# Kernel tuning notes

Hardware: AMD Instinct MI355X
Metric: run time of the kernel (lower is better)

Reference implementation:

```python
import jax, jax.numpy as jnp
import numpy as np

K = 20
EPS = 1e-5
NEG_SLOPE = 0.2


def _graph_feature(x, k):
    # x: [B, N, C] -> edge features [B, N, k, 2C]
    xx = jnp.sum(x * x, axis=-1)                       # [B, N]
    inner = jnp.einsum('bnc,bmc->bnm', x, x)           # [B, N, N]
    neg_dist = 2.0 * inner - xx[:, :, None] - xx[:, None, :]
    idx = jax.lax.top_k(neg_dist, k)[1]                # [B, N, k] nearest neighbors
    nbr = jax.vmap(lambda f, i: f[i])(x, idx)          # [B, N, k, C]
    center = jnp.broadcast_to(x[:, :, None, :], nbr.shape)
    return jnp.concatenate([nbr - center, center], axis=-1)


def _bn(y, gamma, beta, axes):
    mu = y.mean(axes, keepdims=True)
    var = y.var(axes, keepdims=True)
    return (y - mu) * jax.lax.rsqrt(var + EPS) * gamma + beta


def _lrelu(y):
    return jnp.where(y > 0, y, NEG_SLOPE * y)


def _edge_block(feat, w, gamma, beta):
    # feat: [B, N, k, Cin], w: [Cout, Cin] (1x1 conv)
    y = jnp.einsum('bnkc,oc->bnko', feat, w)
    y = _lrelu(_bn(y, gamma, beta, (0, 1, 2)))
    return y.max(axis=2)                               # max over k -> [B, N, Cout]


def setup_inputs() -> dict:
    key = jax.random.key(0)
    ks = jax.random.split(key, 8)
    B, N = 16, 2048
    num_features = 128
    x = jax.random.normal(ks[0], (B, N, 3), dtype=jnp.float32)
    s = 0.05
    w1 = jax.random.normal(ks[1], (64, 6), dtype=jnp.float32) * s
    w2 = jax.random.normal(ks[2], (64, 128), dtype=jnp.float32) * s
    w3 = jax.random.normal(ks[3], (128, 128), dtype=jnp.float32) * s
    w4 = jax.random.normal(ks[4], (256, 256), dtype=jnp.float32) * s
    w5 = jax.random.normal(ks[5], (512, 512), dtype=jnp.float32) * s
    we = jax.random.normal(ks[6], (num_features, 512), dtype=jnp.float32) * s
    def gb(c):
        return jnp.ones((c,), jnp.float32), jnp.zeros((c,), jnp.float32)
    g1, b1 = gb(64); g2, b2 = gb(64); g3, b3 = gb(128); g4, b4 = gb(256); g5, b5 = gb(512)
    return dict(x=x, w1=w1, g1=g1, b1=b1, w2=w2, g2=g2, b2=b2, w3=w3, g3=g3, b3=b3,
                w4=w4, g4=g4, b4=b4, w5=w5, g5=g5, b5=b5, we=we)


def reference(x, w1, g1, b1, w2, g2, b2, w3, g3, b3, w4, g4, b4, w5, g5, b5, we):
    # x: [B, N, 3]
    x1 = _edge_block(_graph_feature(x, K), w1, g1, b1)    # [B, N, 64]
    x2 = _edge_block(_graph_feature(x1, K), w2, g2, b2)   # [B, N, 64]
    x3 = _edge_block(_graph_feature(x2, K), w3, g3, b3)   # [B, N, 128]
    x4 = _edge_block(_graph_feature(x3, K), w4, g4, b4)   # [B, N, 256]
    cat = jnp.concatenate([x1, x2, x3, x4], axis=-1)      # [B, N, 512]
    y = jnp.einsum('bnc,oc->bno', cat, w5)                # conv5 (1x1 conv1d)
    y = _lrelu(_bn(y, g5, b5, (0, 1)))
    y = y.max(axis=1)                                     # global max pool -> [B, 512]
    return y @ we.T                                       # embedding -> [B, num_features]
```

## Files before the change

### kernel.cpp

```cpp
#include <hip/hip_runtime.h>
#include <hip/hip_bf16.h>
#include <cstdint>

#define B_ 16
#define N_ 2048
#define KNN_K 20
#define EPS_ 1e-5f
#define SLOPE_ 0.2f

typedef __attribute__((ext_vector_type(4))) float f32x4;
typedef __attribute__((ext_vector_type(8))) short bf16x8;

static __device__ __forceinline__ float lrelu(float v){ return v > 0.f ? v : SLOPE_*v; }

static __device__ __forceinline__ unsigned encf(float f){
  unsigned b = __float_as_uint(f);
  return (b & 0x80000000u) ? ~b : (b | 0x80000000u);
}
static __device__ __forceinline__ float decf(unsigned u){
  unsigned b = (u & 0x80000000u) ? (u ^ 0x80000000u) : ~u;
  return __uint_as_float(b);
}
static __device__ __forceinline__ short bfbits(float v){
  __hip_bfloat16 h = __float2bfloat16(v);
  return *reinterpret_cast<short*>(&h);
}
static __device__ __forceinline__ float bf2f(short s){
  __hip_bfloat16 h = *reinterpret_cast<__hip_bfloat16*>(&s);
  return __bfloat162float(h);
}

template<int C, int CP>
__global__ __launch_bounds__(256) void convert_kernel(const float* __restrict__ f, int lda,
                                                      short* __restrict__ fbf, size_t plane,
                                                      float* __restrict__ xx){
  int wid  = (blockIdx.x * 256 + threadIdx.x) >> 6;
  int lane = threadIdx.x & 63;
  if (wid >= B_*N_) return;
  const float* p = f + (size_t)wid*lda;
  float s = 0.f;
  for (int c = lane; c < CP; c += 64){
    float v = (c < C) ? p[c] : 0.f;
    short h = bfbits(v);
    float r1 = v - bf2f(h);
    short m = bfbits(r1);
    short l = bfbits(r1 - bf2f(m));
    size_t o = (size_t)wid*CP + c;
    fbf[o] = h;
    fbf[plane + o] = m;
    fbf[2*plane + o] = l;
    s += v*v;
  }
  #pragma unroll
  for (int off=32; off; off>>=1) s += __shfl_down(s, off);
  if (lane==0) xx[wid] = s;
}

template<int CP>
__global__ __launch_bounds__(256, (CP==128)?3:4) void knn_mfma(const short* __restrict__ fbf, size_t plane,
                                                const float* __restrict__ xx,
                                                float* __restrict__ pval, int* __restrict__ pidx){
  constexpr int SP = CP + 8;
  constexpr int CH = CP/8;
  constexpr int KC = CP/32;
  constexpr int PF = 3*CP/32;
  constexpr int FMBS = 3*64*SP;
  constexpr bool ALIAS = (FMBS*2 >= 64*65*4);
  constexpr unsigned LDSB = ALIAS ? (unsigned)(FMBS*2) : (unsigned)(FMBS*2 + 64*65*4);
  __shared__ __align__(16) char ldsbuf[LDSB];
  short* fmb = (short*)ldsbuf;
  float* dtile = ALIAS ? (float*)ldsbuf : (float*)(ldsbuf + FMBS*2);
  __shared__ float xn_s[64], xm_s[64];

  int b   = blockIdx.x >> 6;
  int rem = blockIdx.x & 63;
  int n0  = (rem >> 1) << 6;
  int mh  = rem & 1;
  int mbase = mh << 10;
  int tid = threadIdx.x;
  int w    = tid >> 6;
  int lane = tid & 63;
  int fr = lane & 15, hi = lane >> 4;
  int r_loc = lane >> 2, csub = lane & 3;
  int gb = lane & 60;
  int myrow = w*16 + r_loc;
  size_t browoff = (size_t)b * N_;

  bf16x8 aH[KC], aM[KC], aL[KC];
  {
    size_t arow = (browoff + n0 + w*16 + fr) * (size_t)CP;
    #pragma unroll
    for (int kc=0; kc<KC; ++kc){
      aH[kc] = *(const bf16x8*)&fbf[arow + kc*32 + hi*8];
      aM[kc] = *(const bf16x8*)&fbf[plane + arow + kc*32 + hi*8];
      aL[kc] = *(const bf16x8*)&fbf[2*plane + arow + kc*32 + hi*8];
    }
  }
  if (tid < 64) xn_s[tid] = xx[browoff + n0 + tid];

  float sv[5]; int si[5];
  #pragma unroll
  for (int j=0;j<5;++j){ sv[j] = -1e30f; si[j] = 0x7FFFFFFF; }

  bf16x8 pf[PF];
  float xmreg = 0.f;
  auto PFLOAD = [&](int mt){
    int m0 = mbase + (mt<<6);
    #pragma unroll
    for (int j=0;j<PF;++j){
      int i = tid + j*256;
      int p = i/(64*CH); int rm = i - p*64*CH; int r = rm/CH, cq = rm - r*CH;
      pf[j] = *(const bf16x8*)&fbf[(size_t)p*plane + (browoff + m0 + r)*(size_t)CP + cq*8];
    }
    if (tid < 64) xmreg = xx[browoff + m0 + tid];
  };
  auto WRITEPF = [&](){
    #pragma unroll
    for (int j=0;j<PF;++j){
      int i = tid + j*256;
      int p = i/(64*CH); int rm = i - p*64*CH; int r = rm/CH, cq = rm - r*CH;
      *(bf16x8*)&fmb[p*64*SP + r*SP + cq*8] = pf[j];
    }
    if (tid < 64) xm_s[tid] = xmreg;
  };

  PFLOAD(0);
  WRITEPF();
  __syncthreads();

  for (int mt = 0; mt < 16; ++mt){
    int m0 = mbase + (mt << 6);
    if (mt + 1 < 16) PFLOAD(mt + 1);

    f32x4 acc[4];
    #pragma unroll
    for (int ct=0; ct<4; ++ct) acc[ct] = (f32x4){0.f,0.f,0.f,0.f};
    const short* BH = fmb;
    const short* BM = fmb + 64*SP;
    const short* BL = fmb + 2*64*SP;
    #pragma unroll
    for (int kc = 0; kc < KC; ++kc){
      #pragma unroll
      for (int ct=0; ct<4; ++ct){
        int boff = (ct*16 + fr)*SP + kc*32 + hi*8;
        bf16x8 bh = *(const bf16x8*)&BH[boff];
        bf16x8 bm = *(const bf16x8*)&BM[boff];
        bf16x8 bl = *(const bf16x8*)&BL[boff];
        acc[ct] = __builtin_amdgcn_mfma_f32_16x16x32_bf16(aH[kc], bh, acc[ct], 0,0,0);
        acc[ct] = __builtin_amdgcn_mfma_f32_16x16x32_bf16(aM[kc], bh, acc[ct], 0,0,0);
        acc[ct] = __builtin_amdgcn_mfma_f32_16x16x32_bf16(aH[kc], bm, acc[ct], 0,0,0);
        acc[ct] = __builtin_amdgcn_mfma_f32_16x16x32_bf16(aM[kc], bm, acc[ct], 0,0,0);
        acc[ct] = __builtin_amdgcn_mfma_f32_16x16x32_bf16(aL[kc], bh, acc[ct], 0,0,0);
        acc[ct] = __builtin_amdgcn_mfma_f32_16x16x32_bf16(aH[kc], bl, acc[ct], 0,0,0);
      }
    }
    __syncthreads();

    #pragma unroll
    for (int reg=0; reg<4; ++reg){
      int nl = w*16 + hi*4 + reg;
      float xn = xn_s[nl];
      #pragma unroll
      for (int ct=0; ct<4; ++ct)
        dtile[nl*65 + ct*16 + fr] = 2.f*acc[ct][reg] - xn - xm_s[ct*16 + fr];
    }

    int base = myrow*65 + csub*16;
    float thr = __shfl(sv[4], lane | 3);
    unsigned qm = 0u;
    #pragma unroll
    for (int jj=0; jj<16; ++jj){
      float v = dtile[base + jj];
      qm |= (v > thr) ? (1u << jj) : 0u;
    }
    unsigned long long bal = __ballot(qm != 0u);
    while (bal){
      unsigned nib = (unsigned)((bal >> gb) & 0xFull);
      int leader = nib ? (gb + (int)__builtin_ctz(nib)) : 64;
      int bbit = (int)__builtin_ctz(qm | 0x10000u);
      float mv = dtile[base + (bbit & 15)];
      int mid = m0 + (csub << 4) + bbit;
      float cv = __shfl(mv, leader);
      int   cid = __shfl(mid, leader);
      qm = (lane == leader) ? (qm & (qm - 1u)) : qm;
      int cnt = 0;
      #pragma unroll
      for (int j=0;j<5;++j) cnt += (sv[j] >= cv) ? 1 : 0;
      cnt += __shfl_xor(cnt, 1);
      cnt += __shfl_xor(cnt, 2);
      int pos = nib ? cnt : 20;
      float pv = __shfl_up(sv[4], 1);
      int   pi = __shfl_up(si[4], 1);
      #pragma unroll
      for (int j=0;j<5;++j){
        int g = csub*5 + j;
        float ns = (g < pos) ? sv[j] : ((g == pos) ? cv : pv);
        int   ni = (g < pos) ? si[j] : ((g == pos) ? cid : pi);
        pv = sv[j]; pi = si[j];
        sv[j] = ns; si[j] = ni;
      }
      bal = __ballot(qm != 0u);
    }

    if (mt + 1 < 16){
      if constexpr (ALIAS){
        __syncthreads();
        WRITEPF();
        __syncthreads();
      } else {
        WRITEPF();
        __syncthreads();
      }
    }
  }

  size_t orow = browoff + n0 + myrow;
  float* pvo = pval + (orow*2 + mh)*KNN_K + csub*5;
  int*   pio = pidx + (orow*2 + mh)*KNN_K + csub*5;
  #pragma unroll
  for (int j=0;j<5;++j){ pvo[j] = sv[j]; pio[j] = si[j]; }
}

__global__ __launch_bounds__(256) void knn_merge(const float* __restrict__ pval,
                                                 const int* __restrict__ pidx,
                                                 int* __restrict__ idxout){
  int r = blockIdx.x*256 + threadIdx.x;
  if (r >= B_*N_) return;
  const float* va = pval + (size_t)r*2*KNN_K;
  const float* vb = va + KNN_K;
  const int*   ia = pidx + (size_t)r*2*KNN_K;
  const int*   ib = ia + KNN_K;
  int i=0, j=0;
  #pragma unroll
  for (int t=0;t<KNN_K;++t){
    float a = va[i], bq = vb[j];
    bool ta = (a >= bq);
    idxout[(size_t)r*KNN_K + t] = ta ? ia[i] : ib[j];
    i += ta ? 1 : 0; j += ta ? 0 : 1;
  }
}

template<int CP>
__global__ __launch_bounds__(256) void gemm_pq(const short* __restrict__ fbf, size_t plane,
                                               const float* __restrict__ Wsrc, int wstride, int Cin,
                                               float* __restrict__ Out, int O){
  constexpr int BK = (CP < 64) ? CP : 64;
  constexpr int SP = BK + 8;
  __shared__ short Ah[128*SP];
  __shared__ short Am[128*SP];
  __shared__ short Wh[64*SP];
  __shared__ short Wm[64*SP];
  int obl = O >> 6;
  int bo = ((int)blockIdx.x % obl) << 6;
  int bm = ((int)blockIdx.x / obl) << 7;
  int tid = threadIdx.x;
  int w = tid >> 6, lane = tid & 63;
  int fr = lane & 15, hi = lane >> 4;
  f32x4 acc[2][4];
  #pragma unroll
  for (int g=0; g<2; ++g)
    #pragma unroll
    for (int ct=0; ct<4; ++ct) acc[g][ct] = (f32x4){0.f,0.f,0.f,0.f};

  for (int k0=0; k0<CP; k0+=BK){
    __syncthreads();
    for (int i=tid; i < 128*(BK/8); i += 256){
      int r = i/(BK/8), cq = i%(BK/8);
      size_t src = ((size_t)bm + r)*CP + k0 + cq*8;
      *(bf16x8*)&Ah[r*SP + cq*8] = *(const bf16x8*)&fbf[src];
      *(bf16x8*)&Am[r*SP + cq*8] = *(const bf16x8*)&fbf[plane + src];
    }
    for (int i=tid; i < 64*(BK/8); i += 256){
      int r = i/(BK/8), cq = i%(BK/8);
      bf16x8 vh, vm;
      #pragma unroll
      for (int e=0;e<8;++e){
        int c = k0 + cq*8 + e;
        float v = (c < Cin) ? Wsrc[(size_t)(bo + r)*wstride + c] : 0.f;
        short h = bfbits(v);
        vh[e] = h;
        vm[e] = bfbits(v - bf2f(h));
      }
      *(bf16x8*)&Wh[r*SP + cq*8] = vh;
      *(bf16x8*)&Wm[r*SP + cq*8] = vm;
    }
    __syncthreads();
    #pragma unroll
    for (int kc=0; kc<BK/32; ++kc){
      bf16x8 a0h = *(const bf16x8*)&Ah[(w*32 +      fr)*SP + kc*32 + hi*8];
      bf16x8 a0m = *(const bf16x8*)&Am[(w*32 +      fr)*SP + kc*32 + hi*8];
      bf16x8 a1h = *(const bf16x8*)&Ah[(w*32 + 16 + fr)*SP + kc*32 + hi*8];
      bf16x8 a1m = *(const bf16x8*)&Am[(w*32 + 16 + fr)*SP + kc*32 + hi*8];
      #pragma unroll
      for (int ct=0; ct<4; ++ct){
        bf16x8 bh = *(const bf16x8*)&Wh[(ct*16 + fr)*SP + kc*32 + hi*8];
        bf16x8 bm = *(const bf16x8*)&Wm[(ct*16 + fr)*SP + kc*32 + hi*8];
        acc[0][ct] = __builtin_amdgcn_mfma_f32_16x16x32_bf16(a0h, bh, acc[0][ct], 0,0,0);
        acc[0][ct] = __builtin_amdgcn_mfma_f32_16x16x32_bf16(a0m, bh, acc[0][ct], 0,0,0);
        acc[0][ct] = __builtin_amdgcn_mfma_f32_16x16x32_bf16(a0h, bm, acc[0][ct], 0,0,0);
        acc[1][ct] = __builtin_amdgcn_mfma_f32_16x16x32_bf16(a1h, bh, acc[1][ct], 0,0,0);
        acc[1][ct] = __builtin_amdgcn_mfma_f32_16x16x32_bf16(a1m, bh, acc[1][ct], 0,0,0);
        acc[1][ct] = __builtin_amdgcn_mfma_f32_16x16x32_bf16(a1h, bm, acc[1][ct], 0,0,0);
      }
    }
  }
  #pragma unroll
  for (int g=0; g<2; ++g)
    #pragma unroll
    for (int ct=0; ct<4; ++ct)
      #pragma unroll
      for (int reg=0; reg<4; ++reg){
        int row = bm + w*32 + g*16 + hi*4 + reg;
        Out[(size_t)row*O + bo + ct*16 + fr] = acc[g][ct][reg];
      }
}

__global__ __launch_bounds__(256) void gemm_bf16(const float* __restrict__ A,
                                                 const float* __restrict__ Wt,
                                                 float* __restrict__ C){
  __shared__ short As[128*72];
  __shared__ short Bs[64*72];
  int bm = (int)(blockIdx.x >> 3) << 7;
  int bo = (int)(blockIdx.x & 7) << 6;
  int tid = threadIdx.x;
  int w = tid >> 6, lane = tid & 63;
  int fr = lane & 15, hi = lane >> 4;
  f32x4 acc[2][4];
  #pragma unroll
  for (int g=0; g<2; ++g)
    #pragma unroll
    for (int ct=0; ct<4; ++ct) acc[g][ct] = (f32x4){0.f,0.f,0.f,0.f};

  for (int k0=0; k0<512; k0+=64){
    __syncthreads();
    #pragma unroll 2
    for (int i = tid; i < 1024; i += 256){
      int r = i >> 3, cq = i & 7;
      const float* src = &A[(size_t)(bm + r)*512 + k0 + cq*8];
      bf16x8 v;
      #pragma unroll
      for (int e=0;e<8;++e) v[e] = bfbits(src[e]);
      *(bf16x8*)&As[r*72 + cq*8] = v;
    }
    #pragma unroll 2
    for (int i = tid; i < 512; i += 256){
      int r = i >> 3, cq = i & 7;
      const float* src = &Wt[(size_t)(bo + r)*512 + k0 + cq*8];
      bf16x8 v;
      #pragma unroll
      for (int e=0;e<8;++e) v[e] = bfbits(src[e]);
      *(bf16x8*)&Bs[r*72 + cq*8] = v;
    }
    __syncthreads();
    #pragma unroll
    for (int kc=0; kc<2; ++kc){
      bf16x8 a0 = *(const bf16x8*)&As[(w*32 +      fr)*72 + kc*32 + hi*8];
      bf16x8 a1 = *(const bf16x8*)&As[(w*32 + 16 + fr)*72 + kc*32 + hi*8];
      #pragma unroll
      for (int ct=0; ct<4; ++ct){
        bf16x8 bb = *(const bf16x8*)&Bs[(ct*16 + fr)*72 + kc*32 + hi*8];
        acc[0][ct] = __builtin_amdgcn_mfma_f32_16x16x32_bf16(a0, bb, acc[0][ct], 0,0,0);
        acc[1][ct] = __builtin_amdgcn_mfma_f32_16x16x32_bf16(a1, bb, acc[1][ct], 0,0,0);
      }
    }
  }
  #pragma unroll
  for (int g=0; g<2; ++g)
    #pragma unroll
    for (int ct=0; ct<4; ++ct)
      #pragma unroll
      for (int reg=0; reg<4; ++reg){
        int row = bm + w*32 + g*16 + hi*4 + reg;
        C[(size_t)row*512 + bo + ct*16 + fr] = acc[g][ct][reg];
      }
}

__global__ void wq_kernel(const float* __restrict__ w, float* __restrict__ wq, int Cin, int O){
  int i = blockIdx.x*blockDim.x + threadIdx.x;
  if (i >= O*Cin) return;
  int o = i / Cin, c = i - o*Cin;
  wq[i] = w[(size_t)o*2*Cin + Cin + c] - w[(size_t)o*2*Cin + c];
}

__global__ void zero_f_kernel(float* p, int n){
  int i = blockIdx.x*blockDim.x + threadIdx.x;
  if (i < n) p[i] = 0.f;
}
__global__ void zero_u_kernel(unsigned* p, int n){
  int i = blockIdx.x*blockDim.x + threadIdx.x;
  if (i < n) p[i] = 0u;
}

__global__ __launch_bounds__(256) void edge_agg(const float* __restrict__ P, const float* __restrict__ Q,
      const int* __restrict__ idx, const float* __restrict__ gamma,
      float* __restrict__ S, float* __restrict__ sums, float* __restrict__ sumsq, int O){
  const int ROWS = 64;
  int rpi = 256 / O;
  int iters = ROWS / rpi;
  int row0 = blockIdx.x * ROWS;
  int tid = threadIdx.x;
  int o  = tid % O;
  int rl = tid / O;
  int b  = row0 / N_;
  __shared__ int sidx[4][KNN_K];
  __shared__ float s1[256], s2[256];
  float g = gamma[o];
  float csum=0.f, csumsq=0.f;
  for (int it=0; it<iters; ++it){
    __syncthreads();
    if (tid < KNN_K*rpi) sidx[tid/KNN_K][tid%KNN_K] = idx[(size_t)(row0 + it*rpi)*KNN_K + tid];
    __syncthreads();
    int row = row0 + it*rpi + rl;
    float q = Q[(size_t)row*O + o];
    float mx=-1e30f, mn=1e30f, s=0.f, ss=0.f;
    #pragma unroll
    for (int k=0;k<KNN_K;++k){
      int m = sidx[rl][k];
      float p = P[((size_t)b*N_ + m)*O + o];
      mx = fmaxf(mx,p); mn = fminf(mn,p);
      float y = p + q; s += y; ss += y*y;
    }
    csum += s; csumsq += ss;
    S[(size_t)row*O + o] = (g >= 0.f ? mx : mn) + q;
  }
  s1[tid]=0.f; s2[tid]=0.f;
  __syncthreads();
  atomicAdd(&s1[o], csum); atomicAdd(&s2[o], csumsq);
  __syncthreads();
  if (tid < O){ atomicAdd(&sums[tid], s1[tid]); atomicAdd(&sumsq[tid], s2[tid]); }
}

__global__ void bn_finalize(const float* __restrict__ sums, const float* __restrict__ sumsq,
                            const float* __restrict__ gamma, const float* __restrict__ beta,
                            float invM, float* __restrict__ scale, float* __restrict__ shift, int O){
  int o = blockIdx.x*blockDim.x + threadIdx.x;
  if (o >= O) return;
  float mu = sums[o]*invM;
  float var = sumsq[o]*invM - mu*mu;
  float rs = rsqrtf(var + EPS_);
  float sc = gamma[o]*rs;
  scale[o] = sc; shift[o] = beta[o] - mu*sc;
}

__global__ void apply_write(const float* __restrict__ S, const float* __restrict__ scale,
                            const float* __restrict__ shift, float* __restrict__ cat, int off, int O){
  int i = blockIdx.x*blockDim.x + threadIdx.x;
  if (i >= B_*N_*O) return;
  int row = i / O, o = i - row*O;
  float v = S[i]*scale[o] + shift[o];
  cat[(size_t)row*512 + off + o] = lrelu(v);
}

__global__ __launch_bounds__(256) void conv5_stats(const float* __restrict__ Y, const float* __restrict__ g5,
      float* __restrict__ sums, float* __restrict__ sumsq, unsigned* __restrict__ maxenc){
  int bb = blockIdx.x / 16;
  int n0 = (blockIdx.x % 16) * 128;
  int tid = threadIdx.x;
  float s0=0.f, s1=0.f, q0=0.f, q1=0.f, m0=-1e30f, m1=-1e30f;
  float ga = g5[tid], gb = g5[tid+256];
  for (int n=0;n<128;++n){
    size_t base = ((size_t)bb*N_ + n0 + n)*512;
    float ya = Y[base + tid];
    float yb = Y[base + tid + 256];
    s0 += ya; q0 += ya*ya;
    s1 += yb; q1 += yb*yb;
    m0 = fmaxf(m0, ga>=0.f ? ya : -ya);
    m1 = fmaxf(m1, gb>=0.f ? yb : -yb);
  }
  atomicAdd(&sums[tid],      s0); atomicAdd(&sumsq[tid],      q0);
  atomicAdd(&sums[tid+256],  s1); atomicAdd(&sumsq[tid+256],  q1);
  atomicMax(&maxenc[bb*512 + tid],       encf(m0));
  atomicMax(&maxenc[bb*512 + tid + 256], encf(m1));
}

__global__ void pool_kernel(const unsigned* __restrict__ maxenc, const float* __restrict__ scale,
                            const float* __restrict__ shift, const float* __restrict__ g5,
                            float* __restrict__ pooled){
  int i = blockIdx.x*blockDim.x + threadIdx.x;
  if (i >= B_*512) return;
  int o = i & 511;
  float t = decf(maxenc[i]);
  float y = g5[o] >= 0.f ? t : -t;
  pooled[i] = lrelu(y*scale[o] + shift[o]);
}

__global__ void final_mm(const float* __restrict__ pooled, const float* __restrict__ we,
                         float* __restrict__ out){
  int i = blockIdx.x*blockDim.x + threadIdx.x;
  if (i >= B_*128) return;
  int b = i >> 7, j = i & 127;
  const float4* pp = (const float4*)(pooled + (size_t)b*512);
  const float4* wp = (const float4*)(we + (size_t)j*512);
  float s = 0.f;
  for (int c=0;c<128;++c){
    float4 a = pp[c], w = wp[c];
    s += a.x*w.x + a.y*w.y + a.z*w.z + a.w*w.w;
  }
  out[i] = s;
}

struct Ws {
  float* cat; float* P; float* Q; float* S; int* idx; float* xx;
  float* sums; float* sumsq; float* scale; float* shift;
  float* wq; unsigned* maxenc; float* pooled; short* fbf;
  float* pval; int* pidx;
};

template<int C, int CP>
static void run_layer(const Ws& W, const float* f, int lda, int O,
                      const float* w, const float* g, const float* bt,
                      int off_out, hipStream_t stream){
  const int M = B_*N_;
  size_t plane = (size_t)M*CP;
  convert_kernel<C, CP><<<M/4, 256, 0, stream>>>(f, lda, W.fbf, plane, W.xx);
  knn_mfma<CP><<<B_*(N_/64)*2, 256, 0, stream>>>(W.fbf, plane, W.xx, W.pval, W.pidx);
  knn_merge<<<(M+255)/256, 256, 0, stream>>>(W.pval, W.pidx, W.idx);
  int nwq = O*C;
  wq_kernel<<<(nwq+255)/256, 256, 0, stream>>>(w, W.wq, C, O);
  int grid = (M/128)*(O/64);
  gemm_pq<CP><<<grid, 256, 0, stream>>>(W.fbf, plane, w,    2*C, C, W.P, O);
  gemm_pq<CP><<<grid, 256, 0, stream>>>(W.fbf, plane, W.wq, C,   C, W.Q, O);
  zero_f_kernel<<<4, 256, 0, stream>>>(W.sums, 1024);
  edge_agg<<<M/64, 256, 0, stream>>>(W.P, W.Q, W.idx, g, W.S, W.sums, W.sumsq, O);
  bn_finalize<<<(O+255)/256, 256, 0, stream>>>(W.sums, W.sumsq, g, bt,
                                               1.f/((float)M*KNN_K), W.scale, W.shift, O);
  apply_write<<<(M*O+255)/256, 256, 0, stream>>>(W.S, W.scale, W.shift, W.cat, off_out, O);
}

extern "C" void kernel_launch(void* const* d_in, const int* in_sizes, int n_in,
                              void* d_out, int out_size, void* d_ws, size_t ws_size,
                              hipStream_t stream) {
  const float* x  = (const float*)d_in[0];
  const float* w1 = (const float*)d_in[1];
  const float* g1 = (const float*)d_in[2];
  const float* b1 = (const float*)d_in[3];
  const float* w2 = (const float*)d_in[4];
  const float* g2 = (const float*)d_in[5];
  const float* b2 = (const float*)d_in[6];
  const float* w3 = (const float*)d_in[7];
  const float* g3 = (const float*)d_in[8];
  const float* b3 = (const float*)d_in[9];
  const float* w4 = (const float*)d_in[10];
  const float* g4 = (const float*)d_in[11];
  const float* b4 = (const float*)d_in[12];
  const float* w5 = (const float*)d_in[13];
  const float* g5 = (const float*)d_in[14];
  const float* b5 = (const float*)d_in[15];
  const float* we = (const float*)d_in[16];

  char* ws = (char*)d_ws;
  Ws W;
  size_t off = 0;
  W.cat   = (float*)(ws + off); off += (size_t)16*2048*512*4;
  W.P     = (float*)(ws + off); off += (size_t)16*2048*256*4;
  W.Q     = (float*)(ws + off); off += (size_t)16*2048*256*4;
  W.S     = (float*)(ws + off); off += (size_t)16*2048*256*4;
  W.idx   = (int*)  (ws + off); off += (size_t)16*2048*20*4;
  W.xx    = (float*)(ws + off); off += (size_t)16*2048*4;
  W.sums  = (float*)(ws + off); off += 512*4;
  W.sumsq = (float*)(ws + off); off += 512*4;
  W.scale = (float*)(ws + off); off += 512*4;
  W.shift = (float*)(ws + off); off += 512*4;
  W.wq    = (float*)(ws + off); off += (size_t)256*128*4;
  W.maxenc= (unsigned*)(ws + off); off += (size_t)16*512*4;
  W.pooled= (float*)(ws + off); off += (size_t)16*512*4;
  W.fbf   = (short*)W.S;
  W.pval  = W.Q;
  W.pidx  = (int*)(W.Q + (size_t)2*16*2048*KNN_K);

  const int M = B_*N_;

  run_layer<3,   32>(W, x,           3,   64,  w1, g1, b1, 0,   stream);
  run_layer<64,  64>(W, W.cat,       512, 64,  w2, g2, b2, 64,  stream);
  run_layer<64,  64>(W, W.cat + 64,  512, 128, w3, g3, b3, 128, stream);
  run_layer<128,128>(W, W.cat + 128, 512, 256, w4, g4, b4, 256, stream);

  float* y5 = W.P;
  gemm_bf16<<<(M/128)*8, 256, 0, stream>>>(W.cat, w5, y5);
  zero_f_kernel<<<4, 256, 0, stream>>>(W.sums, 1024);
  zero_u_kernel<<<32, 256, 0, stream>>>(W.maxenc, 16*512);
  conv5_stats<<<B_*16, 256, 0, stream>>>(y5, g5, W.sums, W.sumsq, W.maxenc);
  bn_finalize<<<2, 256, 0, stream>>>(W.sums, W.sumsq, g5, b5, 1.f/(float)M, W.scale, W.shift, 512);
  pool_kernel<<<(16*512+255)/256, 256, 0, stream>>>(W.maxenc, W.scale, W.shift, g5, W.pooled);
  final_mm<<<(16*128+255)/256, 256, 0, stream>>>(W.pooled, we, (float*)d_out);
}
```

Baseline: 1.280 ms.

## Replace 3-way bf16 split with scaled 2-way fp16 split in KNN and GEMM

Switches the split-precision emulation of fp32 dot products from three bf16 planes (six MFMAs per step) to two fp16 planes (three MFMAs per step). The residual plane is scaled by 2048 and accumulated separately, then rescaled when combined. This halves the MFMA work in the KNN distance kernel, cuts one feature plane from memory traffic and LDS, and lets the KNN kernel use higher occupancy. The cost is fp16's narrower range, which risks overflow or underflow on large or tiny activations and could change neighbor selection.

```diff
diff --git a/kernel.cpp b/kernel.cpp
--- a/kernel.cpp
+++ b/kernel.cpp
@@ -7,9 +7,11 @@
 #define KNN_K 20
 #define EPS_ 1e-5f
 #define SLOPE_ 0.2f
+#define IMS 4.8828125e-4f
 
 typedef __attribute__((ext_vector_type(4))) float f32x4;
 typedef __attribute__((ext_vector_type(8))) short bf16x8;
+typedef __attribute__((ext_vector_type(8))) _Float16 f16x8;
 
 static __device__ __forceinline__ float lrelu(float v){ return v > 0.f ? v : SLOPE_*v; }
 
@@ -25,9 +27,13 @@
   __hip_bfloat16 h = __float2bfloat16(v);
   return *reinterpret_cast<short*>(&h);
 }
-static __device__ __forceinline__ float bf2f(short s){
-  __hip_bfloat16 h = *reinterpret_cast<__hip_bfloat16*>(&s);
-  return __bfloat162float(h);
+static __device__ __forceinline__ short h16(float v){
+  _Float16 h = (_Float16)v;
+  return *reinterpret_cast<short*>(&h);
+}
+static __device__ __forceinline__ float h2f(short s){
+  _Float16 h = *reinterpret_cast<_Float16*>(&s);
+  return (float)h;
 }
 
 template<int C, int CP>
@@ -41,14 +47,11 @@
   float s = 0.f;
   for (int c = lane; c < CP; c += 64){
     float v = (c < C) ? p[c] : 0.f;
-    short h = bfbits(v);
-    float r1 = v - bf2f(h);
-    short m = bfbits(r1);
-    short l = bfbits(r1 - bf2f(m));
+    short h = h16(v);
+    short m = h16((v - h2f(h)) * 2048.f);
     size_t o = (size_t)wid*CP + c;
     fbf[o] = h;
     fbf[plane + o] = m;
-    fbf[2*plane + o] = l;
     s += v*v;
   }
   #pragma unroll
@@ -57,14 +60,14 @@
 }
 
 template<int CP>
-__global__ __launch_bounds__(256, (CP==128)?3:4) void knn_mfma(const short* __restrict__ fbf, size_t plane,
+__global__ __launch_bounds__(256, 4) void knn_mfma(const short* __restrict__ fbf, size_t plane,
                                                 const float* __restrict__ xx,
                                                 float* __restrict__ pval, int* __restrict__ pidx){
   constexpr int SP = CP + 8;
   constexpr int CH = CP/8;
   constexpr int KC = CP/32;
-  constexpr int PF = 3*CP/32;
-  constexpr int FMBS = 3*64*SP;
+  constexpr int PF = CP/16;
+  constexpr int FMBS = 2*64*SP;
   constexpr bool ALIAS = (FMBS*2 >= 64*65*4);
   constexpr unsigned LDSB = ALIAS ? (unsigned)(FMBS*2) : (unsigned)(FMBS*2 + 64*65*4);
   __shared__ __align__(16) char ldsbuf[LDSB];
@@ -86,14 +89,13 @@
   int myrow = w*16 + r_loc;
   size_t browoff = (size_t)b * N_;
 
-  bf16x8 aH[KC], aM[KC], aL[KC];
+  f16x8 aH[KC], aM[KC];
   {
     size_t arow = (browoff + n0 + w*16 + fr) * (size_t)CP;
     #pragma unroll
     for (int kc=0; kc<KC; ++kc){
-      aH[kc] = *(const bf16x8*)&fbf[arow + kc*32 + hi*8];
-      aM[kc] = *(const bf16x8*)&fbf[plane + arow + kc*32 + hi*8];
-      aL[kc] = *(const bf16x8*)&fbf[2*plane + arow + kc*32 + hi*8];
+      aH[kc] = *(const f16x8*)&fbf[arow + kc*32 + hi*8];
+      aM[kc] = *(const f16x8*)&fbf[plane + arow + kc*32 + hi*8];
     }
   }
   if (tid < 64) xn_s[tid] = xx[browoff + n0 + tid];
@@ -102,7 +104,7 @@
   #pragma unroll
   for (int j=0;j<5;++j){ sv[j] = -1e30f; si[j] = 0x7FFFFFFF; }
 
-  bf16x8 pf[PF];
+  f16x8 pf[PF];
   float xmreg = 0.f;
   auto PFLOAD = [&](int mt){
     int m0 = mbase + (mt<<6);
@@ -110,7 +112,7 @@
     for (int j=0;j<PF;++j){
       int i = tid + j*256;
       int p = i/(64*CH); int rm = i - p*64*CH; int r = rm/CH, cq = rm - r*CH;
-      pf[j] = *(const bf16x8*)&fbf[(size_t)p*plane + (browoff + m0 + r)*(size_t)CP + cq*8];
+      pf[j] = *(const f16x8*)&fbf[(size_t)p*plane + (browoff + m0 + r)*(size_t)CP + cq*8];
     }
     if (tid < 64) xmreg = xx[browoff + m0 + tid];
   };
@@ -119,7 +121,7 @@
     for (int j=0;j<PF;++j){
       int i = tid + j*256;
       int p = i/(64*CH); int rm = i - p*64*CH; int r = rm/CH, cq = rm - r*CH;
-      *(bf16x8*)&fmb[p*64*SP + r*SP + cq*8] = pf[j];
+      *(f16x8*)&fmb[p*64*SP + r*SP + cq*8] = pf[j];
     }
     if (tid < 64) xm_s[tid] = xmreg;
   };
@@ -132,26 +134,21 @@
     int m0 = mbase + (mt << 6);
     if (mt + 1 < 16) PFLOAD(mt + 1);
 
-    f32x4 acc[4];
-    #pragma unroll
-    for (int ct=0; ct<4; ++ct) acc[ct] = (f32x4){0.f,0.f,0.f,0.f};
+    f32x4 accH[4], accM[4];
+    #pragma unroll
+    for (int ct=0; ct<4; ++ct){ accH[ct] = (f32x4){0.f,0.f,0.f,0.f}; accM[ct] = accH[ct]; }
     const short* BH = fmb;
     const short* BM = fmb + 64*SP;
-    const short* BL = fmb + 2*64*SP;
     #pragma unroll
     for (int kc = 0; kc < KC; ++kc){
       #pragma unroll
       for (int ct=0; ct<4; ++ct){
         int boff = (ct*16 + fr)*SP + kc*32 + hi*8;
-        bf16x8 bh = *(const bf16x8*)&BH[boff];
-        bf16x8 bm = *(const bf16x8*)&BM[boff];
-        bf16x8 bl = *(const bf16x8*)&BL[boff];
-        acc[ct] = __builtin_amdgcn_mfma_f32_16x16x32_bf16(aH[kc], bh, acc[ct], 0,0,0);
-        acc[ct] = __builtin_amdgcn_mfma_f32_16x16x32_bf16(aM[kc], bh, acc[ct], 0,0,0);
-        acc[ct] = __builtin_amdgcn_mfma_f32_16x16x32_bf16(aH[kc], bm, acc[ct], 0,0,0);
-        acc[ct] = __builtin_amdgcn_mfma_f32_16x16x32_bf16(aM[kc], bm, acc[ct], 0,0,0);
-        acc[ct] = __builtin_amdgcn_mfma_f32_16x16x32_bf16(aL[kc], bh, acc[ct], 0,0,0);
-        acc[ct] = __builtin_amdgcn_mfma_f32_16x16x32_bf16(aH[kc], bl, acc[ct], 0,0,0);
+        f16x8 bh = *(const f16x8*)&BH[boff];
+        f16x8 bm = *(const f16x8*)&BM[boff];
+        accH[ct] = __builtin_amdgcn_mfma_f32_16x16x32_f16(aH[kc], bh, accH[ct], 0,0,0);
+        accM[ct] = __builtin_amdgcn_mfma_f32_16x16x32_f16(aM[kc], bh, accM[ct], 0,0,0);
+        accM[ct] = __builtin_amdgcn_mfma_f32_16x16x32_f16(aH[kc], bm, accM[ct], 0,0,0);
       }
     }
     __syncthreads();
@@ -162,7 +159,7 @@
       float xn = xn_s[nl];
       #pragma unroll
       for (int ct=0; ct<4; ++ct)
-        dtile[nl*65 + ct*16 + fr] = 2.f*acc[ct][reg] - xn - xm_s[ct*16 + fr];
+        dtile[nl*65 + ct*16 + fr] = 2.f*(accH[ct][reg] + IMS*accM[ct][reg]) - xn - xm_s[ct*16 + fr];
     }
 
     int base = myrow*65 + csub*16;
@@ -256,51 +253,51 @@
   int tid = threadIdx.x;
   int w = tid >> 6, lane = tid & 63;
   int fr = lane & 15, hi = lane >> 4;
-  f32x4 acc[2][4];
+  f32x4 accH[2][4], accM[2][4];
   #pragma unroll
   for (int g=0; g<2; ++g)
     #pragma unroll
-    for (int ct=0; ct<4; ++ct) acc[g][ct] = (f32x4){0.f,0.f,0.f,0.f};
+    for (int ct=0; ct<4; ++ct){ accH[g][ct] = (f32x4){0.f,0.f,0.f,0.f}; accM[g][ct] = accH[g][ct]; }
 
   for (int k0=0; k0<CP; k0+=BK){
     __syncthreads();
     for (int i=tid; i < 128*(BK/8); i += 256){
       int r = i/(BK/8), cq = i%(BK/8);
       size_t src = ((size_t)bm + r)*CP + k0 + cq*8;
-      *(bf16x8*)&Ah[r*SP + cq*8] = *(const bf16x8*)&fbf[src];
-      *(bf16x8*)&Am[r*SP + cq*8] = *(const bf16x8*)&fbf[plane + src];
+      *(f16x8*)&Ah[r*SP + cq*8] = *(const f16x8*)&fbf[src];
+      *(f16x8*)&Am[r*SP + cq*8] = *(const f16x8*)&fbf[plane + src];
     }
     for (int i=tid; i < 64*(BK/8); i += 256){
       int r = i/(BK/8), cq = i%(BK/8);
-      bf16x8 vh, vm;
+      f16x8 vh, vm;
       #pragma unroll
       for (int e=0;e<8;++e){
         int c = k0 + cq*8 + e;
         float v = (c < Cin) ? Wsrc[(size_t)(bo + r)*wstride + c] : 0.f;
-        short h = bfbits(v);
+        _Float16 h = (_Float16)v;
         vh[e] = h;
-        vm[e] = bfbits(v - bf2f(h));
-      }
-      *(bf16x8*)&Wh[r*SP + cq*8] = vh;
-      *(bf16x8*)&Wm[r*SP + cq*8] = vm;
+        vm[e] = (_Float16)((v - (float)h) * 2048.f);
+      }
+      *(f16x8*)&Wh[r*SP + cq*8] = vh;
+      *(f16x8*)&Wm[r*SP + cq*8] = vm;
     }
     __syncthreads();
     #pragma unroll
     for (int kc=0; kc<BK/32; ++kc){
-      bf16x8 a0h = *(const bf16x8*)&Ah[(w*32 +      fr)*SP + kc*32 + hi*8];
-      bf16x8 a0m = *(const bf16x8*)&Am[(w*32 +      fr)*SP + kc*32 + hi*8];
-      bf16x8 a1h = *(const bf16x8*)&Ah[(w*32 + 16 + fr)*SP + kc*32 + hi*8];
-      bf16x8 a1m = *(const bf16x8*)&Am[(w*32 + 16 + fr)*SP + kc*32 + hi*8];
+      f16x8 a0h = *(const f16x8*)&Ah[(w*32 +      fr)*SP + kc*32 + hi*8];
+      f16x8 a0m = *(const f16x8*)&Am[(w*32 +      fr)*SP + kc*32 + hi*8];
+      f16x8 a1h = *(const f16x8*)&Ah[(w*32 + 16 + fr)*SP + kc*32 + hi*8];
+      f16x8 a1m = *(const f16x8*)&Am[(w*32 + 16 + fr)*SP + kc*32 + hi*8];
       #pragma unroll
       for (int ct=0; ct<4; ++ct){
-        bf16x8 bh = *(const bf16x8*)&Wh[(ct*16 + fr)*SP + kc*32 + hi*8];
-        bf16x8 bm = *(const bf16x8*)&Wm[(ct*16 + fr)*SP + kc*32 + hi*8];
-        acc[0][ct] = __builtin_amdgcn_mfma_f32_16x16x32_bf16(a0h, bh, acc[0][ct], 0,0,0);
-        acc[0][ct] = __builtin_amdgcn_mfma_f32_16x16x32_bf16(a0m, bh, acc[0][ct], 0,0,0);
-        acc[0][ct] = __builtin_amdgcn_mfma_f32_16x16x32_bf16(a0h, bm, acc[0][ct], 0,0,0);
-        acc[1][ct] = __builtin_amdgcn_mfma_f32_16x16x32_bf16(a1h, bh, acc[1][ct], 0,0,0);
-        acc[1][ct] = __builtin_amdgcn_mfma_f32_16x16x32_bf16(a1m, bh, acc[1][ct], 0,0,0);
-        acc[1][ct] = __builtin_amdgcn_mfma_f32_16x16x32_bf16(a1h, bm, acc[1][ct], 0,0,0);
+        f16x8 bh = *(const f16x8*)&Wh[(ct*16 + fr)*SP + kc*32 + hi*8];
+        f16x8 bm = *(const f16x8*)&Wm[(ct*16 + fr)*SP + kc*32 + hi*8];
+        accH[0][ct] = __builtin_amdgcn_mfma_f32_16x16x32_f16(a0h, bh, accH[0][ct], 0,0,0);
+        accM[0][ct] = __builtin_amdgcn_mfma_f32_16x16x32_f16(a0m, bh, accM[0][ct], 0,0,0);
+        accM[0][ct] = __builtin_amdgcn_mfma_f32_16x16x32_f16(a0h, bm, accM[0][ct], 0,0,0);
+        accH[1][ct] = __builtin_amdgcn_mfma_f32_16x16x32_f16(a1h, bh, accH[1][ct], 0,0,0);
+        accM[1][ct] = __builtin_amdgcn_mfma_f32_16x16x32_f16(a1m, bh, accM[1][ct], 0,0,0);
+        accM[1][ct] = __builtin_amdgcn_mfma_f32_16x16x32_f16(a1h, bm, accM[1][ct], 0,0,0);
       }
     }
   }
@@ -311,7 +308,7 @@
       #pragma unroll
       for (int reg=0; reg<4; ++reg){
         int row = bm + w*32 + g*16 + hi*4 + reg;
-        Out[(size_t)row*O + bo + ct*16 + fr] = acc[g][ct][reg];
+        Out[(size_t)row*O + bo + ct*16 + fr] = accH[g][ct][reg] + IMS*accM[g][ct][reg];
       }
 }
 
```

New measurement: 1.201 ms. 1.07x faster.
